# Optimization experiments

Measured on AMD Instinct MI355X. Metric: run time of the kernel, lower is better.

The kernel has to match this reference:

```python
import jax, jax.numpy as jnp
import numpy as np
from jax import lax

EPS = 1e-5

def _bn(x):
    # BatchNorm1d, training-mode batch stats, affine at init (gamma=1, beta=0)
    return (x - x.mean(0)) / jnp.sqrt(x.var(0) + EPS)

def _nonlinear(x, W1, W2):
    h = jax.nn.relu(_bn(x @ W1.T))
    return jax.nn.relu(_bn(h @ W2.T))

def _conv_bn_lrelu(x, w):
    # x: [E, C, L], w: [O, C, 3], padding=1; BN over (batch, length)
    y = lax.conv_general_dilated(x, w, (1,), [(1, 1)], dimension_numbers=('NCH', 'OIH', 'NCH'))
    m = y.mean((0, 2), keepdims=True)
    v = y.var((0, 2), keepdims=True)
    y = (y - m) / jnp.sqrt(v + EPS)
    return jnp.where(y >= 0, y, 0.01 * y)  # LeakyReLU(negative_slope=0.01)

def _curve_encoder(x, c1, c2, c3, fc):
    y = _conv_bn_lrelu(x, c1)
    y = _conv_bn_lrelu(y, c2)
    y = _conv_bn_lrelu(y, c3)
    y = y.mean(-1)            # AdaptiveAvgPool1d(1)
    return _bn(y @ fc.T)      # _fc: Linear(bias=False) + BN, no activation

def _forward(attn_bias, angle, centroid_distance, edge_data, edge_type,
             edge_length, edge_convexity, node_feat,
             sd_emb, virt, angle_W1, angle_W2, cent_W1, cent_W2,
             etype_W1, etype_W2, elen_W1, elen_W2, econv_W1, econv_W2,
             curv_c1, curv_c2, curv_c3, curv_fc, edis_w,
             ec_Wp, ec_W1, ec_W2,
             shortest_distance, edge_path, edge_padding_mask, src, dst):
    B, N, _ = shortest_distance.shape
    H = sd_emb.shape[1]
    D = edge_path.shape[-1]           # multi_hop_max_dist
    n_edge = edge_padding_mask.shape[1]

    bias = jnp.broadcast_to(attn_bias[:, None], (B, H, N + 1, N + 1))

    # shortest-distance / angle / centroid biases, all [B, H, N, N]
    sdb = sd_emb[shortest_distance].transpose(0, 3, 1, 2)
    ang = _nonlinear(angle.reshape(-1, 1), angle_W1, angle_W2).reshape(B, N, N, H).transpose(0, 3, 1, 2)
    cen = _nonlinear(centroid_distance.reshape(-1, 1), cent_W1, cent_W2).reshape(B, N, N, H).transpose(0, 3, 1, 2)

    # --- multi_hop branch ---
    ef = (_curve_encoder(edge_data.transpose(0, 2, 1), curv_c1, curv_c2, curv_c3, curv_fc)
          + _nonlinear(edge_type, etype_W1, etype_W2)
          + _nonlinear(edge_length[:, None], elen_W1, elen_W2)
          + _nonlinear(edge_convexity, econv_W1, econv_W2))     # [E, H]
    # EdgeConv (UV-Net style node_cat): proj(n[src]) + proj(n[dst]) + efeat -> MLP -> BN -> ReLU
    proj = node_feat @ ec_Wp.T
    agg = proj[src] + proj[dst] + ef
    h = jax.nn.relu(_bn(agg @ ec_W1.T)) @ ec_W2.T
    ef2 = jax.nn.relu(_bn(h))                                   # [E, H]

    # edge_padding_mask is all-False, so edge_feature[edge_pos] = ef2 is a plain
    # row-major reshape; slot n_edge stays zero (padding target of edge_path)
    edge_feature = jnp.zeros((B, n_edge + 1, H), dtype=edge_data.dtype)
    edge_feature = edge_feature.at[:, :n_edge].set(ef2.reshape(B, n_edge, H))

    sd_ = jnp.where(shortest_distance == 0, 1, shortest_distance)
    sd_ = jnp.where(sd_ > 1, sd_ - 1, sd_)
    sd_ = jnp.clip(sd_, 0, D)

    ep = edge_path.reshape(B, N * N * D)
    eb = jnp.take_along_axis(edge_feature, ep[:, :, None], axis=1).reshape(B, N, N, D, H)
    Wd = edis_w.reshape(-1, H, H)[:D]                           # [D, H, H]
    eb = jnp.einsum('bijdh,dhk->bijk', eb, Wd)                  # per-hop bmm fused with hop-sum
    eb = eb / (sd_.astype(eb.dtype)[..., None] + 1e-6)
    eb = jnp.nan_to_num(eb)
    ebias = eb.transpose(0, 3, 1, 2)                            # [B, H, N, N]

    bias = bias.at[:, :, 1:, 1:].add(sdb + ang + cen + ebias)
    t = virt.reshape(1, H, 1)
    bias = bias.at[:, :, 1:, 0].add(t)
    bias = bias.at[:, :, 0, :].add(t)
    return bias + attn_bias[:, None]


def setup_inputs() -> dict:
    key = jax.random.key(0)
    ks = iter(jax.random.split(key, 48))
    B, N, H, D = 4, 256, 16, 5
    n_edge, n_pts = 1024, 20
    dim_node, num_distance, num_edge_dis = 256, 512, 128
    E = B * n_edge
    tot_nodes = B * N
    rn = lambda *s: jax.random.normal(next(ks), s, jnp.float32)
    return {
        'attn_bias': rn(B, N + 1, N + 1),
        'shortest_distance': jax.random.randint(next(ks), (B, N, N), 0, num_distance),
        'angle': rn(B, N, N),
        'centroid_distance': rn(B, N, N),
        'edge_path': jax.random.randint(next(ks), (B, N, N, D), 0, n_edge + 1),
        'edge_data': rn(E, n_pts, 12),
        'edge_type': rn(E, 11),
        'edge_length': rn(E),
        'edge_convexity': rn(E, 3),
        'edge_padding_mask': jnp.zeros((B, n_edge), dtype=bool),
        'src': jax.random.randint(next(ks), (E,), 0, tot_nodes),
        'dst': jax.random.randint(next(ks), (E,), 0, tot_nodes),
        'node_feat': rn(tot_nodes, dim_node),
        'sd_emb': (rn(num_distance, H) * 0.02).at[0].set(0.0),  # padding_idx=0
        'virt': rn(1, H) * 0.02,
        'angle_W1': rn(H, 1) * 0.1, 'angle_W2': rn(H, H) * 0.1,
        'cent_W1': rn(H, 1) * 0.1, 'cent_W2': rn(H, H) * 0.1,
        'etype_W1': rn(H, 11) * 0.1, 'etype_W2': rn(H, H) * 0.1,
        'elen_W1': rn(H, 1) * 0.1, 'elen_W2': rn(H, H) * 0.1,
        'econv_W1': rn(H, 3) * 0.1, 'econv_W2': rn(H, H) * 0.1,
        'curv_c1': rn(64, 12, 3) * 0.1, 'curv_c2': rn(128, 64, 3) * 0.05,
        'curv_c3': rn(256, 128, 3) * 0.05, 'curv_fc': rn(H, 256) * 0.05,
        'edis_w': rn(num_edge_dis * H * H, 1) * 0.02,
        'ec_Wp': rn(H, dim_node) * 0.02, 'ec_W1': rn(64, H) * 0.02, 'ec_W2': rn(H, 64) * 0.02,
    }


def reference(attn_bias, shortest_distance, angle, centroid_distance, edge_path,
              edge_data, edge_type, edge_length, edge_convexity, edge_padding_mask,
              src, dst, node_feat, sd_emb, virt, angle_W1, angle_W2, cent_W1, cent_W2,
              etype_W1, etype_W2, elen_W1, elen_W2, econv_W1, econv_W2,
              curv_c1, curv_c2, curv_c3, curv_fc, edis_w, ec_Wp, ec_W1, ec_W2):
    return _forward(attn_bias, angle, centroid_distance, edge_data, edge_type,
                    edge_length, edge_convexity, node_feat,
                    sd_emb, virt, angle_W1, angle_W2, cent_W1, cent_W2,
                    etype_W1, etype_W2, elen_W1, elen_W2, econv_W1, econv_W2,
                    curv_c1, curv_c2, curv_c3, curv_fc, edis_w,
                    ec_Wp, ec_W1, ec_W2,
                    shortest_distance, edge_path, edge_padding_mask, src, dst)
```

## Files before the change

### kernel.cpp

```cpp
#include <hip/hip_runtime.h>

#define EPSB 1e-5f
#define B_ 4
#define N_ 256
#define H_ 16
#define D_ 5
#define E_ 4096
#define M_PAIR (B_*N_*N_)

typedef __attribute__((ext_vector_type(8))) short short8;
typedef __attribute__((ext_vector_type(4))) float f32x4;

enum {
  SO_ANGX = 0,
  SO_CENX = 2,
  SO_MOMA = 16,
  SO_MOMC = 24,
  SO_C1   = 96,  SO_C1Q   = 160,
  SO_C2   = 224, SO_C2Q   = 352,
  SO_C3   = 480, SO_C3Q   = 736,
  SO_FC   = 992, SO_FCQ   = 1008,
  SO_ET1  = 1024, SO_ET1Q = 1040,
  SO_ET2  = 1056, SO_ET2Q = 1072,
  SO_EL1  = 1088, SO_EL1Q = 1104,
  SO_EL2  = 1120, SO_EL2Q = 1136,
  SO_EV1  = 1152, SO_EV1Q = 1168,
  SO_EV2  = 1184, SO_EV2Q = 1200,
  SO_G1   = 1216, SO_G1Q  = 1280,
  SO_G2   = 1344, SO_G2Q  = 1360,
  STATS_FLOATS = 2048
};

static constexpr size_t F_Y13  = 2048;
static constexpr size_t F_Y2   = F_Y13 + 10485760;
static constexpr size_t F_POOL = F_Y2 + 5242880;
static constexpr size_t F_FCB  = F_POOL + 1048576;
static constexpr size_t F_EF   = F_FCB + 65536;
static constexpr size_t F_PROJ = F_EF + 65536;
static constexpr size_t F_Z1EC = F_PROJ + 16384;
static constexpr size_t F_Z2T  = F_Z1EC + 262144;
static constexpr size_t F_G    = F_Z2T + 196608;
static constexpr size_t F_WT2  = F_G + 328000;
static constexpr size_t F_WT3  = F_WT2 + 12288;

__device__ __forceinline__ float waveSum(float v){
  #pragma unroll
  for(int o=32;o;o>>=1) v += __shfl_down(v,o);
  return v;
}

__device__ __forceinline__ ushort f2bf(float f){
  uint u = __float_as_uint(f);
  uint r = (u + 0x7FFF + ((u>>16)&1)) >> 16;
  return (ushort)r;
}
__device__ __forceinline__ float bf2f(ushort u){
  return __uint_as_float(((uint)u)<<16);
}

__device__ __forceinline__ void red32_atomic(float* ws, int so, int soq, float* s, float* q){
  __shared__ float red[4][32];
  int tid=threadIdx.x, lane=tid&63, wid=tid>>6;
  #pragma unroll
  for(int k=0;k<16;k++){
    float rs=waveSum(s[k]), rq=waveSum(q[k]);
    if(lane==0){ red[wid][k]=rs; red[wid][16+k]=rq; }
  }
  __syncthreads();
  if(tid<32){
    float t=red[0][tid]+red[1][tid]+red[2][tid]+red[3][tid];
    atomicAdd(&ws[tid<16 ? so+tid : soq+(tid-16)], t);
  }
}

#define POOL_BYTES 19456

__device__ void dev_conv1(int bid, const float* __restrict__ ed,
    const float* __restrict__ w, float* __restrict__ ws, char* pool){
  float* wsh = (float*)pool;
  float* xs  = wsh + 2368;
  float* reds= xs + 1920;
  float* redq= reds + 256;
  int tid=threadIdx.x;
  for(int i=tid;i<2304;i+=256){ int o=i/36, r=i%36; wsh[o*37+r]=w[i]; }
  int e0=bid*8;
  for(int i=tid;i<1920;i+=256){
    int e=i/240, r=i%240, l=r/12, c=r%12;
    xs[(e*12+c)*20+l]=ed[(size_t)(e0+e)*240+r];
  }
  __syncthreads();
  int o=tid&63, eg=tid>>6;
  ushort* y1=(ushort*)(ws+F_Y13);
  float ssum=0, ssq=0;
  for(int ee=0;ee<2;ee++){
    int e=eg*2+ee;
    float acc[20];
    #pragma unroll
    for(int l=0;l<20;l++) acc[l]=0;
    for(int c=0;c<12;c++){
      float w0=wsh[o*37+c*3], w1=wsh[o*37+c*3+1], w2=wsh[o*37+c*3+2];
      const float* xr=xs+(e*12+c)*20;
      #pragma unroll
      for(int l=0;l<20;l++){
        acc[l]=fmaf(w1,xr[l],acc[l]);
        if(l>0)  acc[l]=fmaf(w0,xr[l-1],acc[l]);
        if(l<19) acc[l]=fmaf(w2,xr[l+1],acc[l]);
      }
    }
    size_t base=((size_t)(e0+e)*20)*64;
    #pragma unroll
    for(int l=0;l<20;l++){
      y1[base+(size_t)l*64+o]=f2bf(acc[l]);
      ssum+=acc[l]; ssq+=acc[l]*acc[l];
    }
  }
  reds[eg*64+o]=ssum; redq[eg*64+o]=ssq;
  __syncthreads();
  if(tid<64){
    atomicAdd(&ws[SO_C1+tid], reds[tid]+reds[64+tid]+reds[128+tid]+reds[192+tid]);
  } else if(tid<128){
    int oo=tid-64;
    atomicAdd(&ws[SO_C1Q+oo], redq[oo]+redq[64+oo]+redq[128+oo]+redq[192+oo]);
  }
}

__device__ void dev_wprep(int bid, const float* __restrict__ c2w,
    const float* __restrict__ c3w, ushort* __restrict__ wt2, ushort* __restrict__ wt3){
  int t = bid*256 + threadIdx.x;
  if(t < 128*192){
    int idx=t;
    int j=idx&7, lane=(idx>>3)&63, ks=(idx>>9)%6, ct=idx/3072;
    int l16=lane&15, lhi=lane>>4;
    int o=ct*16+l16, tap=ks/2, c=(ks%2)*32+lhi*8+j;
    wt2[idx]=f2bf(c2w[(o*64+c)*3+tap]);
  } else {
    int idx=t-128*192;
    if(idx<256*384){
      int j=idx&7, lane=(idx>>3)&63, ks=(idx>>9)%12, ct=idx/6144;
      int l16=lane&15, lhi=lane>>4;
      int o=ct*16+l16, tap=ks/4, c=(ks%4)*32+lhi*8+j;
      wt3[idx]=f2bf(c3w[(o*128+c)*3+tap]);
    }
  }
}

__device__ void dev_proj(int bid, const float* __restrict__ nf,
    const float* __restrict__ Wp, float* __restrict__ ws, char* pool){
  float* wps=(float*)pool;
  int tid=threadIdx.x;
  for(int i=tid;i<4096;i+=256){ wps[(i>>8)*260+(i&255)]=Wp[i]; }
  __syncthreads();
  int t=bid*256+tid;
  int v=t>>4, h=t&15;
  const float4* row=(const float4*)(nf+(size_t)v*256);
  const float4* wr=(const float4*)(wps+h*260);
  float z=0;
  #pragma unroll 8
  for(int c=0;c<64;c++){
    float4 a=row[c], b=wr[c];
    z+=a.x*b.x+a.y*b.y+a.z*b.z+a.w*b.w;
  }
  ws[F_PROJ+t]=z;
}

__device__ void dev_scalar(int bid, const float* __restrict__ ang,
    const float* __restrict__ cen, float* __restrict__ st){
  int tid = bid*256 + threadIdx.x;
  float sa=0, qa=0, sc=0, qc=0;
  for(int i=tid; i<M_PAIR; i += 256*256){
    float a=ang[i], c=cen[i];
    sa+=a; qa+=a*a; sc+=c; qc+=c*c;
  }
  __shared__ float red[4][4];
  int lane=threadIdx.x&63, wid=threadIdx.x>>6;
  sa=waveSum(sa); qa=waveSum(qa); sc=waveSum(sc); qc=waveSum(qc);
  if(lane==0){ red[wid][0]=sa; red[wid][1]=qa; red[wid][2]=sc; red[wid][3]=qc; }
  __syncthreads();
  if(threadIdx.x<4){
    float t=red[0][threadIdx.x]+red[1][threadIdx.x]+red[2][threadIdx.x]+red[3][threadIdx.x];
    atomicAdd(&st[threadIdx.x], t);
  }
}

template<int DIM>
__device__ void dev_sml1(const float* __restrict__ x,
    const float* __restrict__ W1, float* __restrict__ ws, int so, int soq, int bid){
  __shared__ float w1s[176];
  int tid=threadIdx.x;
  if(tid<16*DIM) w1s[tid]=W1[tid];
  __syncthreads();
  int e=bid*256+tid;
  float xv[DIM];
  #pragma unroll
  for(int j=0;j<DIM;j++) xv[j]=x[(size_t)e*DIM+j];
  float s[16], q[16];
  #pragma unroll
  for(int k=0;k<16;k++){
    float z=0;
    #pragma unroll
    for(int j=0;j<DIM;j++) z+=w1s[k*DIM+j]*xv[j];
    s[k]=z; q[k]=z*z;
  }
  red32_atomic(ws, so, soq, s, q);
}

__global__ __launch_bounds__(256) void k_front(
    const float* __restrict__ ed, const float* __restrict__ c1w,
    const float* __restrict__ c2w, const float* __restrict__ c3w,
    const float* __restrict__ nf, const float* __restrict__ Wp,
    const float* __restrict__ ang, const float* __restrict__ cen,
    const float* __restrict__ et, const float* __restrict__ el, const float* __restrict__ ev,
    const float* __restrict__ etW1, const float* __restrict__ elW1, const float* __restrict__ evW1,
    float* __restrict__ ws){
  __shared__ char pool[POOL_BYTES];
  int bx=blockIdx.x;
  if(bx<512)        dev_conv1(bx, ed, c1w, ws, pool);
  else if(bx<992)   dev_wprep(bx-512, c2w, c3w, (ushort*)(ws+F_WT2), (ushort*)(ws+F_WT3));
  else if(bx<1056)  dev_proj(bx-992, nf, Wp, ws, pool);
  else if(bx<1312)  dev_scalar(bx-1056, ang, cen, ws);
  else {
    int bid=bx-1312;
    int g=bid>>4, b2=bid&15;
    if(g==0)      dev_sml1<11>(et,etW1,ws,SO_ET1,SO_ET1Q,b2);
    else if(g==1) dev_sml1<1> (el,elW1,ws,SO_EL1,SO_EL1Q,b2);
    else          dev_sml1<3> (ev,evW1,ws,SO_EV1,SO_EV1Q,b2);
  }
}


__device__ void dev_mom2(int bid, const float* __restrict__ x, float* __restrict__ st,
    int soX, int mo){
  int tid=threadIdx.x;
  float mu = st[soX]*(1.0f/262144.0f);
  float P=0,N=0,Pq=0,Nq=0;
  for(int i=bid*256+tid; i<M_PAIR; i+=32*256){
    float dx=x[i]-mu;
    if(dx>0){ P+=dx; Pq+=dx*dx; } else { N+=dx; Nq+=dx*dx; }
  }
  __shared__ float red[4][4];
  int lane=tid&63, wid=tid>>6;
  P=waveSum(P); N=waveSum(N); Pq=waveSum(Pq); Nq=waveSum(Nq);
  if(lane==0){ red[wid][0]=P; red[wid][1]=N; red[wid][2]=Pq; red[wid][3]=Nq; }
  __syncthreads();
  if(tid<4){
    float t=red[0][tid]+red[1][tid]+red[2][tid]+red[3][tid];
    atomicAdd(&st[mo+tid], t);
  }
}

template<int DIM>
__device__ void dev_sml2(const float* __restrict__ x,
    const float* __restrict__ W1, const float* __restrict__ W2,
    float* __restrict__ ws, int so1, int so1q, int so2, int so2q,
    float* __restrict__ z2out, int bid){
  __shared__ float w1s[176];
  __shared__ float w2s[256];
  __shared__ float mi[16][2];
  int tid=threadIdx.x;
  if(tid<16*DIM) w1s[tid]=W1[tid];
  w2s[tid]=W2[tid];
  if(tid<16){
    float m=ws[so1+tid]*(1.0f/4096.0f);
    float v=ws[so1q+tid]*(1.0f/4096.0f)-m*m; if(v<0)v=0;
    mi[tid][0]=m; mi[tid][1]=rsqrtf(v+EPSB);
  }
  __syncthreads();
  int e=bid*256+tid;
  float xv[DIM];
  #pragma unroll
  for(int j=0;j<DIM;j++) xv[j]=x[(size_t)e*DIM+j];
  float h1[16];
  #pragma unroll
  for(int h=0;h<16;h++){
    float z=0;
    #pragma unroll
    for(int j=0;j<DIM;j++) z+=w1s[h*DIM+j]*xv[j];
    z=(z-mi[h][0])*mi[h][1];
    h1[h]=z>0?z:0;
  }
  float s[16], q[16];
  #pragma unroll
  for(int k=0;k<16;k++){
    float z=0;
    #pragma unroll
    for(int h=0;h<16;h++) z+=w2s[k*16+h]*h1[h];
    z2out[(size_t)e*16+k]=z;
    s[k]=z; q[k]=z*z;
  }
  red32_atomic(ws, so2, so2q, s, q);
}

__global__ __launch_bounds__(256) void k_stats2(
    const float* __restrict__ ang, const float* __restrict__ cen,
    const float* __restrict__ et, const float* __restrict__ el, const float* __restrict__ ev,
    const float* __restrict__ etW1, const float* __restrict__ etW2,
    const float* __restrict__ elW1, const float* __restrict__ elW2,
    const float* __restrict__ evW1, const float* __restrict__ evW2,
    float* __restrict__ ws){
  int bx=blockIdx.x;
  if(bx<32)       dev_mom2(bx, ang, ws, SO_ANGX, SO_MOMA);
  else if(bx<64)  dev_mom2(bx-32, cen, ws, SO_CENX, SO_MOMC);
  else {
    int bid=bx-64;
    int g=bid>>4, b2=bid&15;
    if(g==0)      dev_sml2<11>(et,etW1,etW2,ws,SO_ET1,SO_ET1Q,SO_ET2,SO_ET2Q,ws+F_Z2T,b2);
    else if(g==1) dev_sml2<1> (el,elW1,elW2,ws,SO_EL1,SO_EL1Q,SO_EL2,SO_EL2Q,ws+F_Z2T+65536,b2);
    else          dev_sml2<3> (ev,evW1,evW2,ws,SO_EV1,SO_EV1Q,SO_EV2,SO_EV2Q,ws+F_Z2T+131072,b2);
  }
}

template<int CIN, int OUT, int EPB, int NSPLIT>
__global__ __launch_bounds__(256) void k_convmf(
    const ushort* __restrict__ yin, const ushort* __restrict__ wt,
    ushort* __restrict__ yout, float* __restrict__ ws,
    int soIn, int soInQ, int soOut, int soOutQ)
{
  constexpr int K = CIN*3;
  constexpr int KSTEPS = K/32;
  constexpr int M = EPB*20;
  constexpr int ROWT = M/16;
  constexpr int WCOLT = OUT/(64*NSPLIT);
  constexpr int ROWS = EPB*22;
  constexpr int RB = CIN*2;
  constexpr uint SWZ = RB/16 - 1;
  __shared__ ushort xs[ROWS*CIN];
  __shared__ float mi[CIN][2];
  int tid = threadIdx.x;
  int bx = blockIdx.x;
  int eblk = bx / NSPLIT, split = bx % NSPLIT;
  for(int c=tid; c<CIN; c+=256){
    float m=ws[soIn+c]*(1.0f/81920.0f);
    float v=ws[soInQ+c]*(1.0f/81920.0f)-m*m; if(v<0)v=0;
    mi[c][0]=m; mi[c][1]=rsqrtf(v+EPSB);
  }
  uint* xs32 = (uint*)xs;
  for(int i=tid; i<EPB*2*(CIN/2); i+=256){
    int e=i/(CIN), r=i%(CIN); int lp = (r < CIN/2)? 0:21; int cw = r%(CIN/2);
    xs32[(e*22+lp)*(CIN/2)+cw]=0;
  }
  __syncthreads();
  int e0 = eblk*EPB;
  const ushort* src = yin + (size_t)e0*20*CIN;
  for(int i=tid; i<EPB*20*(CIN/8); i+=256){
    int c8 = i%(CIN/8); int rl = i/(CIN/8);
    int c = c8*8;
    short8 v = *(const short8*)(src + (size_t)rl*CIN + c);
    uint pk[4];
    #pragma unroll
    for(int jj=0;jj<4;jj++){
      float f0 = bf2f((ushort)v[jj*2]);
      float f1 = bf2f((ushort)v[jj*2+1]);
      f0=(f0-mi[c+jj*2  ][0])*mi[c+jj*2  ][1]; f0= f0>=0?f0:0.01f*f0;
      f1=(f1-mi[c+jj*2+1][0])*mi[c+jj*2+1][1]; f1= f1>=0?f1:0.01f*f1;
      pk[jj] = (uint)f2bf(f0) | ((uint)f2bf(f1)<<16);
    }
    int e = rl/20, l=rl%20;
    int row = e*22 + l + 1;
    uint byteoff = (uint)row*RB + (((uint)c*2) ^ (uint)((row&SWZ)<<4));
    *(uint4*)((char*)xs + byteoff) = make_uint4(pk[0],pk[1],pk[2],pk[3]);
  }
  __syncthreads();

  int lane = tid&63, wid = tid>>6;
  int l16 = lane&15, lhi = lane>>4;
  int colbase = (split*4 + wid) * (OUT/(4*NSPLIT));
  f32x4 acc[ROWT][WCOLT];
  #pragma unroll
  for(int m=0;m<ROWT;m++)
    #pragma unroll
    for(int n=0;n<WCOLT;n++) acc[m][n]=(f32x4){0,0,0,0};
  int rowc[ROWT];
  #pragma unroll
  for(int m=0;m<ROWT;m++){ int r=m*16+l16; rowc[m]=(r/20)*22 + (r%20); }
  const ushort* wptile[WCOLT];
  #pragma unroll
  for(int n=0;n<WCOLT;n++)
    wptile[n] = wt + ((size_t)(colbase/16 + n)*KSTEPS)*512 + (size_t)lane*8;

  short8 aF0[ROWT], bF0[WCOLT], aF1[ROWT], bF1[WCOLT];

#define LOADK(ksv, A, B) { \
    int t_=(ksv)/(CIN/32); int c0_=((ksv)%(CIN/32))*32 + lhi*8; \
    _Pragma("unroll") \
    for(int m=0;m<ROWT;m++){ \
      int row_=rowc[m]+t_; \
      uint off_=(uint)row_*RB + (((uint)c0_*2) ^ (uint)((row_&SWZ)<<4)); \
      A[m]=*(const short8*)((char*)xs+off_); } \
    _Pragma("unroll") \
    for(int n=0;n<WCOLT;n++) B[n]=*(const short8*)(wptile[n]+(ksv)*512); }

#define MFMAK(A, B) { \
    _Pragma("unroll") \
    for(int m=0;m<ROWT;m++) \
      _Pragma("unroll") \
      for(int n=0;n<WCOLT;n++) \
        acc[m][n]=__builtin_amdgcn_mfma_f32_16x16x32_bf16(A[m],B[n],acc[m][n],0,0,0); }

  LOADK(0, aF0, bF0);
  #pragma unroll
  for(int kp=0; kp<KSTEPS/2; kp++){
    int ks = kp*2;
    LOADK(ks+1, aF1, bF1);
    MFMAK(aF0, bF0);
    if(ks+2<KSTEPS) LOADK(ks+2, aF0, bF0);
    MFMAK(aF1, bF1);
  }
#undef LOADK
#undef MFMAK

  #pragma unroll
  for(int n=0;n<WCOLT;n++){
    float s=0,q=0;
    #pragma unroll
    for(int m=0;m<ROWT;m++)
      #pragma unroll
      for(int j=0;j<4;j++){ float a=acc[m][n][j]; s+=a; q+=a*a; }
    s += __shfl_xor(s,16); s += __shfl_xor(s,32);
    q += __shfl_xor(q,16); q += __shfl_xor(q,32);
    if(lhi==0){
      int o = colbase+n*16+l16;
      atomicAdd(&ws[soOut+o], s);
      atomicAdd(&ws[soOutQ+o], q);
    }
  }
  ushort* dst = yout + (size_t)eblk*M*OUT;
  #pragma unroll
  for(int m=0;m<ROWT;m++)
    #pragma unroll
    for(int j=0;j<4;j++){
      int R = m*16 + lhi*4 + j;
      #pragma unroll
      for(int n=0;n<WCOLT;n++)
        dst[(size_t)R*OUT + colbase + n*16 + l16] = f2bf(acc[m][n][j]);
    }
}

__global__ __launch_bounds__(256) void k_poolfc(const float* __restrict__ fcw, float* __restrict__ ws){
  __shared__ float ps[16][260];
  __shared__ float red[4][32];
  __shared__ float mo[256][2];
  int tid=threadIdx.x;
  {
    float m=ws[SO_C3+tid]*(1.0f/81920.0f);
    float v=ws[SO_C3Q+tid]*(1.0f/81920.0f)-m*m; if(v<0)v=0;
    mo[tid][0]=m; mo[tid][1]=rsqrtf(v+EPSB);
  }
  __syncthreads();
  int e0=blockIdx.x*16;
  const ushort* y3=(const ushort*)(ws+F_Y13);
  float m=mo[tid][0], inv=mo[tid][1];
  for(int el=0;el<16;el++){
    const ushort* row=y3+((size_t)(e0+el)*20)*256+tid;
    float s=0;
    #pragma unroll
    for(int l=0;l<20;l++){
      float x=(bf2f(row[(size_t)l*256])-m)*inv;
      s += x>=0.f? x : 0.01f*x;
    }
    ps[el][tid]=s*(1.0f/20.0f);
  }
  __syncthreads();
  int e=tid>>4, h=tid&15;
  const float* wr=fcw+(size_t)h*256;
  float z=0;
  for(int c=0;c<256;c++) z+=ps[e][c]*wr[c];
  ws[F_FCB+(size_t)(e0+e)*16+h]=z;
  float s=z, q=z*z;
  #pragma unroll
  for(int o=16;o<64;o<<=1){ s+=__shfl_down(s,o); q+=__shfl_down(q,o); }
  int lane=tid&63, wid=tid>>6;
  if(lane<16){ red[wid][lane]=s; red[wid][16+lane]=q; }
  __syncthreads();
  if(tid<32){
    float v=red[0][tid]+red[1][tid]+red[2][tid]+red[3][tid];
    atomicAdd(&ws[tid<16? SO_FC+tid : SO_FCQ+(tid-16)], v);
  }
}

__device__ __constant__ int EF_BASES[4][2] = {
  {SO_ET2,SO_ET2Q},{SO_EL2,SO_EL2Q},{SO_EV2,SO_EV2Q},{SO_FC,SO_FCQ}
};

__global__ __launch_bounds__(256) void k_aggef(const int* __restrict__ src, const int* __restrict__ dst,
    const float* __restrict__ ecW1, float* __restrict__ ws){
  __shared__ float w1s[64*17];
  __shared__ float mi[4][16][2];
  __shared__ float aLDS[32][17];
  __shared__ float zLDS[64][33];
  __shared__ float reds[4][64], redq[4][64];
  int tid=threadIdx.x;
  for(int i=tid;i<1024;i+=256) w1s[(i>>4)*17+(i&15)]=ecW1[i];
  if(tid<64){
    int g=tid>>4, h=tid&15;
    float m=ws[EF_BASES[g][0]+h]*(1.0f/4096.0f);
    float v=ws[EF_BASES[g][1]+h]*(1.0f/4096.0f)-m*m; if(v<0)v=0;
    mi[g][h][0]=m; mi[g][h][1]=rsqrtf(v+EPSB);
  }
  __syncthreads();
  int e0=blockIdx.x*32;
  for(int it=tid; it<32*16; it+=256){
    int el=it>>4, h=it&15;
    int e=e0+el;
    float z=ws[F_FCB+(size_t)e*16+h];
    float a=(z-mi[3][h][0])*mi[3][h][1];
    #pragma unroll
    for(int g=0;g<3;g++){
      float z2=ws[F_Z2T+(size_t)g*65536+(size_t)e*16+h];
      float r=(z2-mi[g][h][0])*mi[g][h][1];
      a+= r>0?r:0;
    }
    int s=src[e], d=dst[e];
    a+=ws[F_PROJ+(size_t)s*16+h]+ws[F_PROJ+(size_t)d*16+h];
    aLDS[el][h]=a;
  }
  __syncthreads();
  int o=tid&63, elq=tid>>6;
  float s=0,q=0;
  #pragma unroll
  for(int j=0;j<8;j++){
    int el=elq*8+j;
    float z=0;
    #pragma unroll
    for(int h=0;h<16;h++) z+=w1s[o*17+h]*aLDS[el][h];
    zLDS[o][el]=z;
    s+=z; q+=z*z;
  }
  reds[elq][o]=s; redq[elq][o]=q;
  __syncthreads();
  for(int idx=tid; idx<2048; idx+=256){
    int oo=idx>>5, el=idx&31;
    ws[F_Z1EC+(size_t)oo*E_+e0+el]=zLDS[oo][el];
  }
  if(tid<64){
    atomicAdd(&ws[SO_G1+tid], reds[0][tid]+reds[1][tid]+reds[2][tid]+reds[3][tid]);
  } else if(tid<128){
    int oo=tid-64;
    atomicAdd(&ws[SO_G1Q+oo], redq[0][oo]+redq[1][oo]+redq[2][oo]+redq[3][oo]);
  }
}

__global__ __launch_bounds__(256) void k_ec2(const float* __restrict__ ecW2, float* __restrict__ ws){
  __shared__ float w2s[1024];
  __shared__ float mi[64][2];
  int tid=threadIdx.x;
  for(int i=tid;i<1024;i+=256) w2s[i]=ecW2[i];
  if(tid<64){
    float m=ws[SO_G1+tid]*(1.0f/4096.0f);
    float v=ws[SO_G1Q+tid]*(1.0f/4096.0f)-m*m; if(v<0)v=0;
    mi[tid][0]=m; mi[tid][1]=rsqrtf(v+EPSB);
  }
  __syncthreads();
  int el=tid&63, kq=tid>>6;
  int e=blockIdx.x*64+el;
  float acc[4]={0,0,0,0};
  #pragma unroll 8
  for(int o=0;o<64;o++){
    float z=ws[F_Z1EC+(size_t)o*E_+e];
    float h=(z-mi[o][0])*mi[o][1];
    h=h>0?h:0;
    #pragma unroll
    for(int j=0;j<4;j++) acc[j]+=w2s[(kq*4+j)*64+o]*h;
  }
  #pragma unroll
  for(int j=0;j<4;j++) ws[F_FCB+(size_t)e*16+kq*4+j]=acc[j];
  #pragma unroll
  for(int j=0;j<4;j++){
    float rs=waveSum(acc[j]);
    float rq=waveSum(acc[j]*acc[j]);
    if(el==0){
      atomicAdd(&ws[SO_G2+kq*4+j], rs);
      atomicAdd(&ws[SO_G2Q+kq*4+j], rq);
    }
  }
}

__global__ __launch_bounds__(256) void k_ef2g(const float* __restrict__ edisw, float* __restrict__ ws){
  __shared__ float wd[1280];
  __shared__ float mi[16][2];
  int tid=threadIdx.x;
  for(int i=tid;i<1280;i+=256) wd[i]=edisw[i];
  if(tid<16){
    float m=ws[SO_G2+tid]*(1.0f/4096.0f);
    float va=ws[SO_G2Q+tid]*(1.0f/4096.0f)-m*m; if(va<0)va=0;
    mi[tid][0]=m; mi[tid][1]=rsqrtf(va+EPSB);
  }
  __syncthreads();
  int t=blockIdx.x*256+tid;
  if(t>=4*1025*5) return;
  int bp=t/5, d=t%5;
  int b=bp/1025, pos=bp%1025;
  float ef[16];
  if(pos<1024){
    int e=b*1024+pos;
    #pragma unroll
    for(int k=0;k<16;k++){
      float z=ws[F_FCB+(size_t)e*16+k];
      float v=(z-mi[k][0])*mi[k][1];
      ef[k]= v>0?v:0;
    }
  } else {
    #pragma unroll
    for(int k=0;k<16;k++) ef[k]=0;
  }
  float* g=ws+F_G+(size_t)bp*80+d*16;
  const float* wdd=wd+d*256;
  #pragma unroll
  for(int k=0;k<16;k++){
    float s=0;
    #pragma unroll
    for(int h=0;h<16;h++) s+=ef[h]*wdd[h*16+k];
    g[k]=s;
  }
}

__global__ __launch_bounds__(256) void k_pair(const float* __restrict__ ab,
    const int* __restrict__ sd, const float* __restrict__ ang, const float* __restrict__ cen,
    const int* __restrict__ ep, const float* __restrict__ sdemb,
    const float* __restrict__ angW1, const float* __restrict__ angW2,
    const float* __restrict__ cenW1, const float* __restrict__ cenW2,
    const float* __restrict__ ws, float* __restrict__ out){
  __shared__ float cpa[16],cma[16],m2a[16],i2a[16];
  __shared__ float cpc[16],cmc[16],m2c[16],i2c[16];
  __shared__ float mv[4];
  int tid=threadIdx.x;
  if(tid==0){
    float s=ws[SO_ANGX], q=ws[SO_ANGX+1];
    float mu=s*(1.0f/262144.0f);
    float v=q*(1.0f/262144.0f)-mu*mu; if(v<0)v=0;
    mv[0]=mu; mv[1]=v;
    s=ws[SO_CENX]; q=ws[SO_CENX+1];
    mu=s*(1.0f/262144.0f);
    v=q*(1.0f/262144.0f)-mu*mu; if(v<0)v=0;
    mv[2]=mu; mv[3]=v;
  }
  __syncthreads();
  if(tid<32){
    int k=tid&15; bool isC = tid>=16;
    const float* W1=isC?cenW1:angW1; const float* W2=isC?cenW2:angW2;
    float var=isC?mv[3]:mv[1];
    float cp=0, cm=0;
    for(int h=0;h<16;h++){
      float w=W1[h];
      float A=w*rsqrtf(var*w*w+EPSB);
      float wk=W2[k*16+h];
      if(A>0) cp+=wk*A; else cm+=wk*A;
    }
    int mo = isC? SO_MOMC : SO_MOMA;
    float P=ws[mo], N=ws[mo+1], Pq=ws[mo+2], Nq=ws[mo+3];
    float mean=(cp*P+cm*N)*(1.0f/262144.0f);
    float e2=(cp*cp*Pq+cm*cm*Nq)*(1.0f/262144.0f);
    float v2=e2-mean*mean; if(v2<0)v2=0;
    float iv=rsqrtf(v2+EPSB);
    if(!isC){ cpa[k]=cp; cma[k]=cm; m2a[k]=mean; i2a[k]=iv; }
    else    { cpc[k]=cp; cmc[k]=cm; m2c[k]=mean; i2c[k]=iv; }
  }
  __syncthreads();
  int t=blockIdx.x*256+tid;
  int b=t>>16, rem=t&65535, i=rem>>8, j=rem&255;
  int sdv=sd[t];
  float xa=ang[t], xc0=cen[t];
  float acc[16];
  const float* se=sdemb+(size_t)sdv*16;
  #pragma unroll
  for(int k=0;k<16;k++) acc[k]=se[k];
  {
    float dx=xa-mv[0];
    bool pos=dx>0.f;
    #pragma unroll
    for(int k=0;k<16;k++){
      float z=dx*(pos?cpa[k]:cma[k]);
      float r=(z-m2a[k])*i2a[k];
      acc[k]+= r>0?r:0;
    }
  }
  {
    float dx=xc0-mv[2];
    bool pos=dx>0.f;
    #pragma unroll
    for(int k=0;k<16;k++){
      float z=dx*(pos?cpc[k]:cmc[k]);
      float r=(z-m2c[k])*i2c[k];
      acc[k]+= r>0?r:0;
    }
  }
  {
    int sdm = sdv==0 ? 1 : sdv;
    if(sdm>1) sdm-=1;
    if(sdm>5) sdm=5;
    float inv=1.0f/((float)sdm+1e-6f);
    float eb[16];
    #pragma unroll
    for(int k=0;k<16;k++) eb[k]=0;
    const float* G=ws+F_G;
    #pragma unroll
    for(int d=0;d<5;d++){
      int idx=ep[(size_t)t*5+d];
      const float4* g=(const float4*)(G+(size_t)(b*1025+idx)*80+d*16);
      float4 g0=g[0], g1=g[1], g2=g[2], g3=g[3];
      eb[0]+=g0.x; eb[1]+=g0.y; eb[2]+=g0.z; eb[3]+=g0.w;
      eb[4]+=g1.x; eb[5]+=g1.y; eb[6]+=g1.z; eb[7]+=g1.w;
      eb[8]+=g2.x; eb[9]+=g2.y; eb[10]+=g2.z; eb[11]+=g2.w;
      eb[12]+=g3.x; eb[13]+=g3.y; eb[14]+=g3.z; eb[15]+=g3.w;
    }
    #pragma unroll
    for(int k=0;k<16;k++) acc[k]+=eb[k]*inv;
  }
  float base2=2.0f*ab[(size_t)b*66049+(size_t)(i+1)*257+(j+1)];
  #pragma unroll
  for(int k=0;k<16;k++)
    out[(((size_t)b*16+k)*257+(i+1))*257+(j+1)]=acc[k]+base2;
}

__global__ __launch_bounds__(256) void k_border(const float* __restrict__ ab,
    const float* __restrict__ virt, float* __restrict__ out){
  int t=blockIdx.x*256+threadIdx.x;
  if(t>=4*16*513) return;
  int idx=t%513, bh=t/513;
  int b=bh>>4, h=bh&15;
  float v=virt[h];
  if(idx<257){
    out[(((size_t)b*16+h)*257)*257+idx]=2.0f*ab[(size_t)b*66049+idx]+v;
  } else {
    int p=idx-256;
    out[(((size_t)b*16+h)*257+p)*257]=2.0f*ab[(size_t)b*66049+(size_t)p*257]+v;
  }
}

extern "C" void kernel_launch(void* const* d_in, const int* in_sizes, int n_in,
                              void* d_out, int out_size, void* d_ws, size_t ws_size,
                              hipStream_t stream) {
  const float* ab    =(const float*)d_in[0];
  const int*   sdist =(const int*)  d_in[1];
  const float* ang   =(const float*)d_in[2];
  const float* cen   =(const float*)d_in[3];
  const int*   ep    =(const int*)  d_in[4];
  const float* edata =(const float*)d_in[5];
  const float* etype =(const float*)d_in[6];
  const float* elen  =(const float*)d_in[7];
  const float* econv =(const float*)d_in[8];
  const int*   src   =(const int*)  d_in[10];
  const int*   dst   =(const int*)  d_in[11];
  const float* nf    =(const float*)d_in[12];
  const float* sdemb =(const float*)d_in[13];
  const float* virt  =(const float*)d_in[14];
  const float* angW1 =(const float*)d_in[15];
  const float* angW2 =(const float*)d_in[16];
  const float* cenW1 =(const float*)d_in[17];
  const float* cenW2 =(const float*)d_in[18];
  const float* etW1  =(const float*)d_in[19];
  const float* etW2  =(const float*)d_in[20];
  const float* elW1  =(const float*)d_in[21];
  const float* elW2  =(const float*)d_in[22];
  const float* evW1  =(const float*)d_in[23];
  const float* evW2  =(const float*)d_in[24];
  const float* c1w   =(const float*)d_in[25];
  const float* c2w   =(const float*)d_in[26];
  const float* c3w   =(const float*)d_in[27];
  const float* fcw   =(const float*)d_in[28];
  const float* edisw =(const float*)d_in[29];
  const float* ecWp  =(const float*)d_in[30];
  const float* ecW1  =(const float*)d_in[31];
  const float* ecW2  =(const float*)d_in[32];
  float* ws=(float*)d_ws;
  float* out=(float*)d_out;

  hipMemsetAsync(d_ws, 0, STATS_FLOATS*sizeof(float), stream);

  k_front<<<1360,256,0,stream>>>(edata,c1w,c2w,c3w,nf,ecWp,ang,cen,
                                 etype,elen,econv,etW1,elW1,evW1,ws);
  k_stats2<<<112,256,0,stream>>>(ang,cen,etype,elen,econv,
                                 etW1,etW2,elW1,elW2,evW1,evW2,ws);

  k_convmf<64,128,4,1><<<1024,256,0,stream>>>((const ushort*)(ws+F_Y13),(const ushort*)(ws+F_WT2),
                                              (ushort*)(ws+F_Y2),ws,SO_C1,SO_C1Q,SO_C2,SO_C2Q);
  k_convmf<128,256,4,2><<<2048,256,0,stream>>>((const ushort*)(ws+F_Y2),(const ushort*)(ws+F_WT3),
                                               (ushort*)(ws+F_Y13),ws,SO_C2,SO_C2Q,SO_C3,SO_C3Q);
  k_poolfc<<<256,256,0,stream>>>(fcw,ws);

  k_aggef<<<128,256,0,stream>>>(src,dst,ecW1,ws);
  k_ec2<<<64,256,0,stream>>>(ecW2,ws);
  k_ef2g<<<81,256,0,stream>>>(edisw,ws);

  k_pair<<<1024,256,0,stream>>>(ab,sdist,ang,cen,ep,sdemb,angW1,angW2,cenW1,cenW2,ws,out);
  k_border<<<129,256,0,stream>>>(ab,virt,out);
}
```

Before: 215.5 us.

## Split conv1 out of front kernel and preload conv weights into registers

Moves conv1 out of the fused front kernel into its own kernel and shrinks the remaining misc kernel's shared pool. In the MFMA conv kernels, each wave now owns a single 16-column output tile, with every weight fragment for all K steps loaded into registers up front. To keep that tiling, the column split doubles, which doubles the grid for both conv2 and conv3. The aim is to remove weight loads from the inner loop and raise parallelism, at the cost of restaging and renormalising the input tile in more blocks, plus one extra kernel launch.

```diff
diff --git a/kernel.cpp b/kernel.cpp
--- a/kernel.cpp
+++ b/kernel.cpp
@@ -73,17 +73,14 @@
   }
 }
 
-#define POOL_BYTES 19456
-
-__device__ void dev_conv1(int bid, const float* __restrict__ ed,
-    const float* __restrict__ w, float* __restrict__ ws, char* pool){
-  float* wsh = (float*)pool;
-  float* xs  = wsh + 2368;
-  float* reds= xs + 1920;
-  float* redq= reds + 256;
+__global__ __launch_bounds__(256) void k_conv1(const float* __restrict__ ed,
+    const float* __restrict__ w, float* __restrict__ ws){
+  __shared__ float wsh[64*37];
+  __shared__ float xs[8*12*20];
+  __shared__ float reds[256], redq[256];
   int tid=threadIdx.x;
   for(int i=tid;i<2304;i+=256){ int o=i/36, r=i%36; wsh[o*37+r]=w[i]; }
-  int e0=bid*8;
+  int e0=blockIdx.x*8;
   for(int i=tid;i<1920;i+=256){
     int e=i/240, r=i%240, l=r/12, c=r%12;
     xs[(e*12+c)*20+l]=ed[(size_t)(e0+e)*240+r];
@@ -123,6 +120,7 @@
     atomicAdd(&ws[SO_C1Q+oo], redq[oo]+redq[64+oo]+redq[128+oo]+redq[192+oo]);
   }
 }
+
 
 __device__ void dev_wprep(int bid, const float* __restrict__ c2w,
     const float* __restrict__ c3w, ushort* __restrict__ wt2, ushort* __restrict__ wt3){
@@ -204,22 +202,20 @@
   red32_atomic(ws, so, soq, s, q);
 }
 
-__global__ __launch_bounds__(256) void k_front(
-    const float* __restrict__ ed, const float* __restrict__ c1w,
+__global__ __launch_bounds__(256) void k_misc(
     const float* __restrict__ c2w, const float* __restrict__ c3w,
     const float* __restrict__ nf, const float* __restrict__ Wp,
     const float* __restrict__ ang, const float* __restrict__ cen,
     const float* __restrict__ et, const float* __restrict__ el, const float* __restrict__ ev,
     const float* __restrict__ etW1, const float* __restrict__ elW1, const float* __restrict__ evW1,
     float* __restrict__ ws){
-  __shared__ char pool[POOL_BYTES];
+  __shared__ char pool[16640];
   int bx=blockIdx.x;
-  if(bx<512)        dev_conv1(bx, ed, c1w, ws, pool);
-  else if(bx<992)   dev_wprep(bx-512, c2w, c3w, (ushort*)(ws+F_WT2), (ushort*)(ws+F_WT3));
-  else if(bx<1056)  dev_proj(bx-992, nf, Wp, ws, pool);
-  else if(bx<1312)  dev_scalar(bx-1056, ang, cen, ws);
+  if(bx<480)       dev_wprep(bx, c2w, c3w, (ushort*)(ws+F_WT2), (ushort*)(ws+F_WT3));
+  else if(bx<544)  dev_proj(bx-480, nf, Wp, ws, pool);
+  else if(bx<800)  dev_scalar(bx-544, ang, cen, ws);
   else {
-    int bid=bx-1312;
+    int bid=bx-800;
     int g=bid>>4, b2=bid&15;
     if(g==0)      dev_sml1<11>(et,etW1,ws,SO_ET1,SO_ET1Q,b2);
     else if(g==1) dev_sml1<1> (el,elW1,ws,SO_EL1,SO_EL1Q,b2);
@@ -319,7 +315,6 @@
   constexpr int KSTEPS = K/32;
   constexpr int M = EPB*20;
   constexpr int ROWT = M/16;
-  constexpr int WCOLT = OUT/(64*NSPLIT);
   constexpr int ROWS = EPB*22;
   constexpr int RB = CIN*2;
   constexpr uint SWZ = RB/16 - 1;
@@ -328,6 +323,15 @@
   int tid = threadIdx.x;
   int bx = blockIdx.x;
   int eblk = bx / NSPLIT, split = bx % NSPLIT;
+  int lane = tid&63, wid = tid>>6;
+  int l16 = lane&15, lhi = lane>>4;
+  int colbase = (split*4 + wid) * 16;
+
+  const ushort* wp = wt + ((size_t)(colbase>>4)*KSTEPS)*512 + (size_t)lane*8;
+  short8 bF[KSTEPS];
+  #pragma unroll
+  for(int ks=0;ks<KSTEPS;ks++) bF[ks]=*(const short8*)(wp + (size_t)ks*512);
+
   for(int c=tid; c<CIN; c+=256){
     float m=ws[soIn+c]*(1.0f/81920.0f);
     float v=ws[soInQ+c]*(1.0f/81920.0f)-m*m; if(v<0)v=0;
@@ -361,64 +365,49 @@
   }
   __syncthreads();
 
-  int lane = tid&63, wid = tid>>6;
-  int l16 = lane&15, lhi = lane>>4;
-  int colbase = (split*4 + wid) * (OUT/(4*NSPLIT));
-  f32x4 acc[ROWT][WCOLT];
-  #pragma unroll
-  for(int m=0;m<ROWT;m++)
-    #pragma unroll
-    for(int n=0;n<WCOLT;n++) acc[m][n]=(f32x4){0,0,0,0};
+  f32x4 acc[ROWT];
+  #pragma unroll
+  for(int m=0;m<ROWT;m++) acc[m]=(f32x4){0,0,0,0};
   int rowc[ROWT];
   #pragma unroll
   for(int m=0;m<ROWT;m++){ int r=m*16+l16; rowc[m]=(r/20)*22 + (r%20); }
-  const ushort* wptile[WCOLT];
-  #pragma unroll
-  for(int n=0;n<WCOLT;n++)
-    wptile[n] = wt + ((size_t)(colbase/16 + n)*KSTEPS)*512 + (size_t)lane*8;
-
-  short8 aF0[ROWT], bF0[WCOLT], aF1[ROWT], bF1[WCOLT];
-
-#define LOADK(ksv, A, B) { \
+
+  short8 aF0[ROWT], aF1[ROWT];
+
+#define LOADA(ksv, A) { \
     int t_=(ksv)/(CIN/32); int c0_=((ksv)%(CIN/32))*32 + lhi*8; \
     _Pragma("unroll") \
     for(int m=0;m<ROWT;m++){ \
       int row_=rowc[m]+t_; \
       uint off_=(uint)row_*RB + (((uint)c0_*2) ^ (uint)((row_&SWZ)<<4)); \
-      A[m]=*(const short8*)((char*)xs+off_); } \
-    _Pragma("unroll") \
-    for(int n=0;n<WCOLT;n++) B[n]=*(const short8*)(wptile[n]+(ksv)*512); }
-
-#define MFMAK(A, B) { \
+      A[m]=*(const short8*)((char*)xs+off_); } }
+
+#define MFMAK(A, ksv) { \
     _Pragma("unroll") \
     for(int m=0;m<ROWT;m++) \
-      _Pragma("unroll") \
-      for(int n=0;n<WCOLT;n++) \
-        acc[m][n]=__builtin_amdgcn_mfma_f32_16x16x32_bf16(A[m],B[n],acc[m][n],0,0,0); }
-
-  LOADK(0, aF0, bF0);
+      acc[m]=__builtin_amdgcn_mfma_f32_16x16x32_bf16(A[m],bF[ksv],acc[m],0,0,0); }
+
+  LOADA(0, aF0);
   #pragma unroll
   for(int kp=0; kp<KSTEPS/2; kp++){
-    int ks = kp*2;
-    LOADK(ks+1, aF1, bF1);
-    MFMAK(aF0, bF0);
-    if(ks+2<KSTEPS) LOADK(ks+2, aF0, bF0);
-    MFMAK(aF1, bF1);
-  }
-#undef LOADK
+    LOADA(kp*2+1, aF1);
+    MFMAK(aF0, kp*2);
+    if(kp*2+2<KSTEPS) LOADA(kp*2+2, aF0);
+    MFMAK(aF1, kp*2+1);
+  }
+#undef LOADA
 #undef MFMAK
 
-  #pragma unroll
-  for(int n=0;n<WCOLT;n++){
+  {
     float s=0,q=0;
     #pragma unroll
     for(int m=0;m<ROWT;m++)
       #pragma unroll
-      for(int j=0;j<4;j++){ float a=acc[m][n][j]; s+=a; q+=a*a; }
+      for(int j=0;j<4;j++){ float a=acc[m][j]; s+=a; q+=a*a; }
     s += __shfl_xor(s,16); s += __shfl_xor(s,32);
     q += __shfl_xor(q,16); q += __shfl_xor(q,32);
     if(lhi==0){
-      int o = colbase+n*16+l16;
+      int o = colbase+l16;
       atomicAdd(&ws[soOut+o], s);
       atomicAdd(&ws[soOutQ+o], q);
     }
@@ -429,9 +418,7 @@
     #pragma unroll
     for(int j=0;j<4;j++){
       int R = m*16 + lhi*4 + j;
-      #pragma unroll
-      for(int n=0;n<WCOLT;n++)
-        dst[(size_t)R*OUT + colbase + n*16 + l16] = f2bf(acc[m][n][j]);
+      dst[(size_t)R*OUT + colbase + l16] = f2bf(acc[m][j]);
     }
 }
 
@@ -766,14 +753,15 @@
 
   hipMemsetAsync(d_ws, 0, STATS_FLOATS*sizeof(float), stream);
 
-  k_front<<<1360,256,0,stream>>>(edata,c1w,c2w,c3w,nf,ecWp,ang,cen,
-                                 etype,elen,econv,etW1,elW1,evW1,ws);
+  k_conv1<<<512,256,0,stream>>>(edata,c1w,ws);
+  k_misc<<<848,256,0,stream>>>(c2w,c3w,nf,ecWp,ang,cen,
+                               etype,elen,econv,etW1,elW1,evW1,ws);
   k_stats2<<<112,256,0,stream>>>(ang,cen,etype,elen,econv,
                                  etW1,etW2,elW1,elW2,evW1,evW2,ws);
 
-  k_convmf<64,128,4,1><<<1024,256,0,stream>>>((const ushort*)(ws+F_Y13),(const ushort*)(ws+F_WT2),
+  k_convmf<64,128,4,2><<<2048,256,0,stream>>>((const ushort*)(ws+F_Y13),(const ushort*)(ws+F_WT2),
                                               (ushort*)(ws+F_Y2),ws,SO_C1,SO_C1Q,SO_C2,SO_C2Q);
-  k_convmf<128,256,4,2><<<2048,256,0,stream>>>((const ushort*)(ws+F_Y2),(const ushort*)(ws+F_WT3),
+  k_convmf<128,256,4,4><<<4096,256,0,stream>>>((const ushort*)(ws+F_Y2),(const ushort*)(ws+F_WT3),
                                                (ushort*)(ws+F_Y13),ws,SO_C2,SO_C2Q,SO_C3,SO_C3Q);
   k_poolfc<<<256,256,0,stream>>>(fcw,ws);
 
```

Measured after the change: 207.0 us. 1.04x faster.
